# Kernel optimization log

Measured on AMD Instinct MI355X. Metric: run time of the kernel, lower is better.

Reference implementation:

```python
import jax, jax.numpy as jnp
import numpy as np

EPS = 1e-6      # vnn EPS used in norms / leaky-relu denominators
BN_EPS = 1e-5   # torch BatchNorm eps
K = 20          # args.n_knn


def vnlin(W, x):
    # VNLinear: apply (O,C) weight over channel axis 1 of x (B,C,3,...)
    return jnp.moveaxis(jnp.tensordot(W, x, axes=((1,), (1,))), 0, 1)


def vn_bn(x):
    # VNBatchNorm (training-mode batch stats, affine = identity init):
    # normalizes the per-vector norms, rescales vectors accordingly.
    norm = jnp.sqrt(jnp.sum(x * x, axis=2)) + EPS        # (B,C,...)
    axes = (0,) + tuple(range(2, norm.ndim))             # per-channel stats
    mean = jnp.mean(norm, axis=axes, keepdims=True)
    var = jnp.var(norm, axis=axes, keepdims=True)
    norm_bn = (norm - mean) / jnp.sqrt(var + BN_EPS)
    return x / jnp.expand_dims(norm, 2) * jnp.expand_dims(norm_bn, 2)


def vn_lrelu(Wf, Wd, x):
    # VNLinearLeakyReLU with negative_slope=0 (as constructed in this module)
    p = vn_bn(vnlin(Wf, x))
    d = vnlin(Wd, x)
    dot = jnp.sum(p * d, axis=2, keepdims=True)
    dsq = jnp.sum(d * d, axis=2, keepdims=True)
    return jnp.where(dot >= 0, p, p - (dot / (dsq + EPS)) * d)


def vn_maxpool(Wd, x):
    # VNMaxPool: pool over last axis, picking per (b,c) the vector maximizing <x,d>
    d = vnlin(Wd, x)
    dot = jnp.sum(x * d, axis=2, keepdims=True)          # (B,C,1,...)
    idx = jnp.argmax(dot, axis=-1)                       # (B,C,1,...)
    idx = jnp.broadcast_to(idx[..., None], x.shape[:-1] + (1,))
    return jnp.take_along_axis(x, idx, axis=-1)[..., 0]


def graph_feature_cross(x, k):
    # x: (B,3,N) -> (B, 3ch, 3vec, N, k); channels = [nbr-x, x, cross(nbr,x)]
    xx = jnp.sum(x * x, axis=1)                          # (B,N)
    inner = jnp.einsum('bdi,bdj->bij', x, x)             # (B,N,N)
    pd = 2.0 * inner - xx[:, :, None] - xx[:, None, :]   # = -||xi-xj||^2
    idx = jax.lax.top_k(pd, k)[1]                        # (B,N,k) nearest
    pts = jnp.swapaxes(x, 1, 2)                          # (B,N,3)
    nb = jax.vmap(lambda p, i: p[i])(pts, idx)           # (B,N,k,3) gather
    c = jnp.broadcast_to(pts[:, :, None, :], nb.shape)   # center repeated
    cross = jnp.cross(nb, c)
    feat = jnp.stack([nb - c, c, cross], axis=3)         # (B,N,k,3,3)
    return jnp.transpose(feat, (0, 3, 4, 1, 2))


_W_SPECS = {
    'pos_Wf': (21, 3), 'pos_Wd': (21, 3), 'pool_Wd': (21, 21),
    'c1_Wf': (21, 21), 'c1_Wd': (21, 21),
    'st1_Wf': (21, 21), 'st1_Wd': (21, 21),
    'st2_Wf': (42, 21), 'st2_Wd': (42, 21),
    'st3_Wf': (341, 42), 'st3_Wd': (341, 42),
    'st_pool_Wd': (341, 341),
    'stf1_Wf': (170, 341), 'stf1_Wd': (170, 341),
    'stf2_Wf': (85, 170), 'stf2_Wd': (85, 170),
    'stf3_W': (21, 85),
    'c2_Wf': (42, 42), 'c2_Wd': (42, 42),
    'c3_W': (341, 42),
    'std1_Wf': (341, 682), 'std1_Wd': (341, 682),
    'std2_Wf': (170, 341), 'std2_Wd': (170, 341),
    'std_lin': (3, 170),
}


def setup_inputs() -> dict:
    key = jax.random.key(0)
    ks = iter(jax.random.split(key, 32))
    inp = {'x': jax.random.normal(next(ks), (8, 3, 4096), dtype=jnp.float32)}
    for name, (o, i) in _W_SPECS.items():
        inp[name] = jax.random.normal(next(ks), (o, i), dtype=jnp.float32) / np.sqrt(i).astype(np.float32)
    return inp


def _forward(x, pos_Wf, pos_Wd, pool_Wd, c1_Wf, c1_Wd, st1_Wf, st1_Wd, st2_Wf, st2_Wd,
             st3_Wf, st3_Wd, st_pool_Wd, stf1_Wf, stf1_Wd, stf2_Wf, stf2_Wd, stf3_W,
             c2_Wf, c2_Wd, c3_W, std1_Wf, std1_Wd, std2_Wf, std2_Wd, std_lin):
    B, D, N = x.shape
    feat = graph_feature_cross(x, K)                     # (B,3,3,N,k)
    h = vn_lrelu(pos_Wf, pos_Wd, feat)                   # (B,21,3,N,k)
    h = vn_maxpool(pool_Wd, h)                           # (B,21,3,N) pool over k
    h = vn_lrelu(c1_Wf, c1_Wd, h)                        # (B,21,3,N)
    # STNkd feature transform
    s = vn_lrelu(st1_Wf, st1_Wd, h)                      # (B,21,3,N)
    s = vn_lrelu(st2_Wf, st2_Wd, s)                      # (B,42,3,N)
    s = vn_lrelu(st3_Wf, st3_Wd, s)                      # (B,341,3,N)
    s = vn_maxpool(st_pool_Wd, s)                        # (B,341,3) pool over N
    s = vn_lrelu(stf1_Wf, stf1_Wd, s)                    # (B,170,3)
    s = vn_lrelu(stf2_Wf, stf2_Wd, s)                    # (B,85,3)
    s = vnlin(stf3_W, s)                                 # (B,21,3)
    s = jnp.broadcast_to(s[..., None], h.shape)          # repeat over N
    h = jnp.concatenate([h, s], axis=1)                  # (B,42,3,N)
    h = vn_lrelu(c2_Wf, c2_Wd, h)                        # (B,42,3,N)
    h = vn_bn(vnlin(c3_W, h))                            # (B,341,3,N)
    h_mean = jnp.broadcast_to(jnp.mean(h, axis=-1, keepdims=True), h.shape)
    h = jnp.concatenate([h, h_mean], axis=1)             # (B,682,3,N)
    # VNStdFeature (normalize_frame=False)
    z0 = vn_lrelu(std1_Wf, std1_Wd, h)                   # (B,341,3,N)
    z0 = vn_lrelu(std2_Wf, std2_Wd, z0)                  # (B,170,3,N)
    z0 = vnlin(std_lin, z0)                              # (B,3,3,N)
    h_std = jnp.einsum('bijm,bjkm->bikm', h, z0)         # (B,682,3,N)
    out = jnp.max(h_std.reshape(B, -1, N), axis=-1)      # (B,2046)
    return out, z0


def reference(x, pos_Wf, pos_Wd, pool_Wd, c1_Wf, c1_Wd, st1_Wf, st1_Wd, st2_Wf, st2_Wd,
              st3_Wf, st3_Wd, st_pool_Wd, stf1_Wf, stf1_Wd, stf2_Wf, stf2_Wd, stf3_W,
              c2_Wf, c2_Wd, c3_W, std1_Wf, std1_Wd, std2_Wf, std2_Wd, std_lin):
    return _forward(x, pos_Wf, pos_Wd, pool_Wd, c1_Wf, c1_Wd, st1_Wf, st1_Wd, st2_Wf,
                    st2_Wd, st3_Wf, st3_Wd, st_pool_Wd, stf1_Wf, stf1_Wd, stf2_Wf,
                    stf2_Wd, stf3_W, c2_Wf, c2_Wd, c3_W, std1_Wf, std1_Wd, std2_Wf,
                    std2_Wd, std_lin)
```

## Files before the change

kernel.cpp:

```cpp
#include <hip/hip_runtime.h>
#include <cstdint>
#include <cstddef>


typedef unsigned short u16;
using bh8  = __attribute__((ext_vector_type(8))) short;
using f32x4 = __attribute__((ext_vector_type(4))) float;

__device__ __forceinline__ float b2f(u16 v) {
  return __uint_as_float(((unsigned)v) << 16);
}
__device__ __forceinline__ u16 f2b(float f) {
  unsigned u = __float_as_uint(f);
  u += 0x7FFFu + ((u >> 16) & 1u);
  return (u16)(u >> 16);
}

__device__ __forceinline__ float ldg(const float* p, size_t i) { return p[i]; }
__device__ __forceinline__ float ldg(const u16* p, size_t i) { return b2f(p[i]); }
__device__ __forceinline__ void st4(float* p, size_t i, float a, float b, float c, float d) {
  float4 v; v.x = a; v.y = b; v.z = c; v.w = d; *(float4*)(p + i) = v;
}

#define FMA4(A, S, V) { A.x += (S)*(V).x; A.y += (S)*(V).y; A.z += (S)*(V).z; A.w += (S)*(V).w; }

__device__ __forceinline__ unsigned long long packKey(float v, int n) {
  unsigned u = __float_as_uint(v);
  u = (u & 0x80000000u) ? ~u : (u | 0x80000000u);
  return ((unsigned long long)u << 32) | (unsigned long long)(0xFFFFFFFFu - (unsigned)n);
}

#define CSWAP(T) { if (c > T) { unsigned long long tmp = T; T = c; c = tmp; } }
__global__ __launch_bounds__(256) void knn_kernel(const float* __restrict__ x,
                                                  int* __restrict__ idxOut, int N) {
  int b = blockIdx.y;
  int wv = threadIdx.x >> 6, lane = threadIdx.x & 63;
  int i = blockIdx.x * 4 + wv;
  const float* xb = x + (size_t)b * 3 * N;
  float xi0 = xb[i], xi1 = xb[N + i], xi2 = xb[2 * (size_t)N + i];
  float xxi = xi0 * xi0 + xi1 * xi1 + xi2 * xi2;
  unsigned long long t0 = 0, t1 = 0, t2 = 0, t3 = 0, t4 = 0, t5 = 0, t6 = 0, t7 = 0;
  #pragma unroll 8
  for (int s = 0; s < 64; ++s) {
    int j = s * 64 + lane;
    float a0 = xb[j], a1 = xb[N + j], a2 = xb[2 * (size_t)N + j];
    float inner = xi0 * a0 + xi1 * a1 + xi2 * a2;
    float xxj = a0 * a0 + a1 * a1 + a2 * a2;
    float pd = 2.f * inner - xxi - xxj;
    unsigned long long c = packKey(pd, j);
    if (c > t7) { CSWAP(t0) CSWAP(t1) CSWAP(t2) CSWAP(t3) CSWAP(t4) CSWAP(t5) CSWAP(t6) CSWAP(t7) }
  }
  int* row = idxOut + ((size_t)b * N + i) * 20;
  for (int kk = 0; kk < 20; ++kk) {
    unsigned long long k = t0;
    #pragma unroll
    for (int off = 1; off < 64; off <<= 1) {
      unsigned long long o = __shfl_xor(k, off);
      if (o > k) k = o;
    }
    if (lane == 0) row[kk] = (int)(0xFFFFFFFFu - (unsigned)(k & 0xFFFFFFFFull));
    if (k == t0) { t0 = t1; t1 = t2; t2 = t3; t3 = t4; t4 = t5; t5 = t6; t6 = t7; t7 = 0; }
  }
}
#undef CSWAP

__global__ __launch_bounds__(256) void pos_stats(const float* __restrict__ x,
                                                 const int* __restrict__ idx,
                                                 const float* __restrict__ Wf,
                                                 float* __restrict__ statSum,
                                                 float* __restrict__ statSq, int N) {
  __shared__ float wf[64];
  __shared__ float part[4][42];
  int tid = threadIdx.x;
  if (tid < 63) wf[tid] = Wf[tid];
  __syncthreads();
  int b = blockIdx.y;
  int lin = blockIdx.x * 256 + tid;
  int n = lin / 20, kk = lin - n * 20;
  const float* xb = x + (size_t)b * 3 * N;
  int j = idx[((size_t)b * N + n) * 20 + kk];
  float c0 = xb[n], c1 = xb[N + n], c2 = xb[2 * (size_t)N + n];
  float a0 = xb[j], a1 = xb[N + j], a2 = xb[2 * (size_t)N + j];
  float e00 = a0 - c0, e01 = a1 - c1, e02 = a2 - c2;
  float e20 = a1 * c2 - a2 * c1, e21 = a2 * c0 - a0 * c2, e22 = a0 * c1 - a1 * c0;
  int lane = tid & 63, wave = tid >> 6;
  #pragma unroll
  for (int c = 0; c < 21; ++c) {
    float w0 = wf[c * 3], w1 = wf[c * 3 + 1], w2 = wf[c * 3 + 2];
    float p0 = w0 * e00 + w1 * c0 + w2 * e20;
    float p1 = w0 * e01 + w1 * c1 + w2 * e21;
    float p2 = w0 * e02 + w1 * c2 + w2 * e22;
    float nr = sqrtf(p0 * p0 + p1 * p1 + p2 * p2) + 1e-6f;
    float u1 = nr, u2 = nr * nr;
    #pragma unroll
    for (int off = 32; off; off >>= 1) { u1 += __shfl_down(u1, off); u2 += __shfl_down(u2, off); }
    if (lane == 0) { part[wave][c] = u1; part[wave][21 + c] = u2; }
  }
  __syncthreads();
  if (tid < 42) {
    float t = part[0][tid] + part[1][tid] + part[2][tid] + part[3][tid];
    if (tid < 21) atomicAdd(&statSum[tid], t);
    else atomicAdd(&statSq[tid - 21], t);
  }
}

__global__ __launch_bounds__(64) void pos_apply(const float* __restrict__ x,
                                                const int* __restrict__ idx,
                                                const float* __restrict__ Wf,
                                                const float* __restrict__ Wd,
                                                const float* __restrict__ Wpool,
                                                const float* __restrict__ statMean,
                                                const float* __restrict__ statIstd,
                                                float* __restrict__ h0, int N) {
  __shared__ float wpool[441];
  __shared__ float hbuf[64];
  int tid = threadIdx.x;
  for (int l = tid; l < 441; l += 64) wpool[l] = Wpool[l];
  int b = blockIdx.y, n = blockIdx.x;
  bool act = tid < 63;
  int c = act ? tid / 3 : 0;
  int v = act ? tid - c * 3 : 0;
  const float* xb = x + (size_t)b * 3 * N;
  float c0 = xb[n], c1 = xb[N + n], c2 = xb[2 * (size_t)N + n];
  float wf0 = 0, wf1 = 0, wf2 = 0, wd0 = 0, wd1 = 0, wd2 = 0, mn = 0, is = 1.f;
  if (act) {
    wf0 = Wf[c * 3]; wf1 = Wf[c * 3 + 1]; wf2 = Wf[c * 3 + 2];
    wd0 = Wd[c * 3]; wd1 = Wd[c * 3 + 1]; wd2 = Wd[c * 3 + 2];
    mn = statMean[c]; is = statIstd[c];
  }
  __syncthreads();
  float best = -3.4e38f, bh = 0.f;
  const int* idxRow = idx + ((size_t)b * N + n) * 20;
  for (int kk = 0; kk < 20; ++kk) {
    int j = idxRow[kk];
    float a0 = xb[j], a1 = xb[N + j], a2 = xb[2 * (size_t)N + j];
    float av  = (v == 0) ? a0 : ((v == 1) ? a1 : a2);
    float cv  = (v == 0) ? c0 : ((v == 1) ? c1 : c2);
    float a1v = (v == 0) ? a1 : ((v == 1) ? a2 : a0);
    float a2v = (v == 0) ? a2 : ((v == 1) ? a0 : a1);
    float c1v = (v == 0) ? c1 : ((v == 1) ? c2 : c0);
    float c2v = (v == 0) ? c2 : ((v == 1) ? c0 : c1);
    float e0 = av - cv;
    float e1 = cv;
    float e2 = a1v * c2v - a2v * c1v;
    float p = wf0 * e0 + wf1 * e1 + wf2 * e2;
    float d = wd0 * e0 + wd1 * e1 + wd2 * e2;
    int base = c * 3;
    float pp = p * p;
    float n2 = __shfl(pp, base) + __shfl(pp, base + 1) + __shfl(pp, base + 2);
    float nr = sqrtf(n2) + 1e-6f;
    float sc = ((nr - mn) * is) / nr;
    float pb = p * sc;
    float pd2 = pb * d, dd = d * d;
    float dot = __shfl(pd2, base) + __shfl(pd2, base + 1) + __shfl(pd2, base + 2);
    float dsq = __shfl(dd, base) + __shfl(dd, base + 1) + __shfl(dd, base + 2);
    float h = (dot >= 0.f) ? pb : pb - (dot / (dsq + 1e-6f)) * d;
    hbuf[tid] = act ? h : 0.f;
    __syncthreads();
    float d2 = 0.f;
    #pragma unroll 7
    for (int cc = 0; cc < 21; ++cc) d2 += wpool[c * 21 + cc] * hbuf[cc * 3 + v];
    float hd = h * d2;
    float dotp = __shfl(hd, base) + __shfl(hd, base + 1) + __shfl(hd, base + 2);
    if (act && dotp > best) { best = dotp; bh = h; }
    __syncthreads();
  }
  if (act) h0[(((size_t)b * 21 + c) * 3 + v) * N + n] = bh;
}

template<int MODE, int CPT, typename TX, typename TY>
__global__ __launch_bounds__(256) void gemm_vn(
    const float* __restrict__ Wf,
    const TX* __restrict__ X, TY* __restrict__ Y,
    float* __restrict__ statSum, float* __restrict__ statSq,
    const float* __restrict__ statMean, const float* __restrict__ statIstd,
    int Cin, int Cout, int CoutStride, int wstride, int N) {
  __shared__ float Xs[16][3][64];
  __shared__ float Wfs[16 * CPT][17];
  const int tid = threadIdx.x;
  const int tx = tid & 15, ty = tid >> 4;
  const int b = blockIdx.z;
  const int n0 = blockIdx.x * 64;
  const int co0 = blockIdx.y * (16 * CPT);
  const TX* Xb = X + (size_t)b * Cin * 3 * N;

  float4 acc[CPT][3];
  #pragma unroll
  for (int c = 0; c < CPT; ++c)
    #pragma unroll
    for (int v = 0; v < 3; ++v) acc[c][v] = {0.f, 0.f, 0.f, 0.f};

  for (int k0 = 0; k0 < Cin; k0 += 16) {
    #pragma unroll
    for (int l0 = 0; l0 < 12; ++l0) {
      int l = l0 * 256 + tid;
      int n = l & 63, v = (l >> 6) % 3, kk = l / 192;
      int ci = k0 + kk;
      Xs[kk][v][n] = (ci < Cin) ? ldg(Xb, ((size_t)ci * 3 + v) * N + n0 + n) : 0.f;
    }
    {
      int kk = tid & 15, coL = tid >> 4, ci = k0 + kk;
      #pragma unroll
      for (int c = 0; c < CPT; ++c) {
        int co = co0 + coL + 16 * c;
        bool ok = (co < Cout) && (ci < Cin);
        Wfs[coL + 16 * c][kk] = ok ? Wf[(size_t)co * wstride + ci] : 0.f;
      }
    }
    __syncthreads();
    #pragma unroll
    for (int kk = 0; kk < 16; ++kk) {
      float4 x0 = *(const float4*)&Xs[kk][0][tx * 4];
      float4 x1 = *(const float4*)&Xs[kk][1][tx * 4];
      float4 x2 = *(const float4*)&Xs[kk][2][tx * 4];
      #pragma unroll
      for (int c = 0; c < CPT; ++c) {
        float w = Wfs[ty + 16 * c][kk];
        FMA4(acc[c][0], w, x0); FMA4(acc[c][1], w, x1); FMA4(acc[c][2], w, x2);
      }
    }
    __syncthreads();
  }

  #pragma unroll
  for (int c = 0; c < CPT; ++c) {
    int co = co0 + ty + 16 * c;
    float p_[3][4];
    #pragma unroll
    for (int v = 0; v < 3; ++v) {
      const float* av = (const float*)&acc[c][v];
      p_[v][0] = av[0]; p_[v][1] = av[1]; p_[v][2] = av[2]; p_[v][3] = av[3];
    }
    if constexpr (MODE == 5) {
      float s1 = 0.f, s2 = 0.f;
      if (co < Cout) {
        size_t yb = ((size_t)b * CoutStride + co) * 3 * N + n0 + tx * 4;
        #pragma unroll
        for (int j = 0; j < 4; ++j) {
          float nr = sqrtf(p_[0][j]*p_[0][j] + p_[1][j]*p_[1][j] + p_[2][j]*p_[2][j]) + 1e-6f;
          s1 += nr; s2 += nr * nr;
        }
        st4(Y, yb,                 p_[0][0], p_[0][1], p_[0][2], p_[0][3]);
        st4(Y, yb + N,             p_[1][0], p_[1][1], p_[1][2], p_[1][3]);
        st4(Y, yb + 2 * (size_t)N, p_[2][0], p_[2][1], p_[2][2], p_[2][3]);
      }
      #pragma unroll
      for (int off = 8; off; off >>= 1) { s1 += __shfl_down(s1, off); s2 += __shfl_down(s2, off); }
      if (tx == 0 && co < Cout) { atomicAdd(&statSum[co], s1); atomicAdd(&statSq[co], s2); }
    } else if constexpr (MODE == 6) {
      if (co < Cout) {
        float mn = statMean[co], is = statIstd[co];
        size_t yb = ((size_t)b * CoutStride + co) * 3 * N + n0 + tx * 4;
        float4 P0 = *(const float4*)&Y[yb];
        float4 P1 = *(const float4*)&Y[yb + N];
        float4 P2 = *(const float4*)&Y[yb + 2 * (size_t)N];
        float pr[3][4] = {{P0.x,P0.y,P0.z,P0.w},{P1.x,P1.y,P1.z,P1.w},{P2.x,P2.y,P2.z,P2.w}};
        float o_[3][4];
        #pragma unroll
        for (int j = 0; j < 4; ++j) {
          float q0 = pr[0][j], q1 = pr[1][j], q2 = pr[2][j];
          float e0 = p_[0][j], e1 = p_[1][j], e2 = p_[2][j];
          float nr = sqrtf(q0*q0 + q1*q1 + q2*q2) + 1e-6f;
          float sc = ((nr - mn) * is) / nr;
          q0 *= sc; q1 *= sc; q2 *= sc;
          float dot = q0*e0 + q1*e1 + q2*e2;
          if (dot < 0.f) {
            float dsq = e0*e0 + e1*e1 + e2*e2;
            float t = dot / (dsq + 1e-6f);
            q0 -= t*e0; q1 -= t*e1; q2 -= t*e2;
          }
          o_[0][j] = q0; o_[1][j] = q1; o_[2][j] = q2;
        }
        st4(Y, yb,                 o_[0][0], o_[0][1], o_[0][2], o_[0][3]);
        st4(Y, yb + N,             o_[1][0], o_[1][1], o_[1][2], o_[1][3]);
        st4(Y, yb + 2 * (size_t)N, o_[2][0], o_[2][1], o_[2][2], o_[2][3]);
      }
    }
  }
}

__global__ __launch_bounds__(256) void gemm_pool_db(
    const float* __restrict__ Wp, const float* __restrict__ Xp,
    unsigned long long* __restrict__ poolPart, int Cout, int N) {
  constexpr int KP = 352, CPT = 4;
  __shared__ float Xs[2][16][3][64];
  __shared__ float Wfs[2][16 * CPT][16];
  const int tid = threadIdx.x;
  const int tx = tid & 15, ty = tid >> 4;
  const int lane = tid & 63, w = tid >> 6;
  const int b = blockIdx.z;
  const int n0 = blockIdx.x * 64;
  const int co0 = blockIdx.y * (16 * CPT);
  const float* Xb = Xp + (size_t)b * KP * 3 * N;

  auto stage = [&](int k0, int buf) {
    #pragma unroll
    for (int l0 = 0; l0 < 12; ++l0) {
      int q = l0 * 4 + w;
      int vv = q % 3, kk = q / 3;
      const float* g = Xb + ((size_t)(k0 + kk) * 3 + vv) * N + n0 + lane;
      __builtin_amdgcn_global_load_lds(
          (const __attribute__((address_space(1))) float*)g,
          (__attribute__((address_space(3))) float*)&Xs[buf][kk][vv][0], 4, 0, 0);
    }
    #pragma unroll
    for (int c = 0; c < CPT; ++c) {
      const float* g = Wp + (size_t)(co0 + w * 4 + (lane >> 4) + 16 * c) * KP + k0 + (lane & 15);
      __builtin_amdgcn_global_load_lds(
          (const __attribute__((address_space(1))) float*)g,
          (__attribute__((address_space(3))) float*)&Wfs[buf][w * 4 + 16 * c][0], 4, 0, 0);
    }
  };

  float4 acc[CPT][3];
  #pragma unroll
  for (int c = 0; c < CPT; ++c)
    #pragma unroll
    for (int v = 0; v < 3; ++v) acc[c][v] = {0.f, 0.f, 0.f, 0.f};

  stage(0, 0);
  __syncthreads();
  constexpr int KT = KP / 16;
  for (int kt = 0; kt < KT; ++kt) {
    int buf = kt & 1;
    if (kt + 1 < KT) stage((kt + 1) * 16, buf ^ 1);
    #pragma unroll
    for (int kk = 0; kk < 16; ++kk) {
      float4 x0 = *(const float4*)&Xs[buf][kk][0][tx * 4];
      float4 x1 = *(const float4*)&Xs[buf][kk][1][tx * 4];
      float4 x2 = *(const float4*)&Xs[buf][kk][2][tx * 4];
      #pragma unroll
      for (int c = 0; c < CPT; ++c) {
        float wv = Wfs[buf][ty + 16 * c][kk];
        FMA4(acc[c][0], wv, x0); FMA4(acc[c][1], wv, x1); FMA4(acc[c][2], wv, x2);
      }
    }
    __syncthreads();
  }

  #pragma unroll
  for (int c = 0; c < CPT; ++c) {
    int co = co0 + ty + 16 * c;
    unsigned long long key = 0;
    if (co < Cout) {
      const float* av0 = (const float*)&acc[c][0];
      const float* av1 = (const float*)&acc[c][1];
      const float* av2 = (const float*)&acc[c][2];
      size_t xb2 = ((size_t)co * 3) * N + n0 + tx * 4;
      #pragma unroll
      for (int j = 0; j < 4; ++j) {
        float X0 = Xb[xb2 + j];
        float X1 = Xb[xb2 + N + j];
        float X2 = Xb[xb2 + 2 * (size_t)N + j];
        float dot = X0 * av0[j] + X1 * av1[j] + X2 * av2[j];
        unsigned long long k2 = packKey(dot, n0 + tx * 4 + j);
        if (k2 > key) key = k2;
      }
    }
    #pragma unroll
    for (int off = 8; off; off >>= 1) {
      unsigned long long o = __shfl_down(key, off);
      if (o > key) key = o;
    }
    if (tx == 0 && co < Cout) poolPart[((size_t)b * Cout + co) * 64 + blockIdx.x] = key;
  }
}

template<int MODE, int NS>
__global__ __launch_bounds__(256) void mfma2(
    const u16* __restrict__ W, const u16* __restrict__ Xt,
    u16* __restrict__ P, float* __restrict__ Zout,
    const float* __restrict__ biasP, const float* __restrict__ biasD,
    float* __restrict__ statSum, float* __restrict__ statSq,
    const float* __restrict__ statMean, const float* __restrict__ statIstd,
    int Cout, int Cpad, int Kpad, int N) {
  const int tid = threadIdx.x, lane = tid & 63, w = tid >> 6;
  const int quad = lane >> 4, l16 = lane & 15;
  const int b = blockIdx.z, n0 = blockIdx.x * 64, co0 = blockIdx.y * 64;
  const int n = n0 + w * 16 + l16;
  const u16* Xb = Xt + (size_t)b * 3 * N * Kpad;
  f32x4 acc[NS][3];
  #pragma unroll
  for (int s = 0; s < NS; ++s)
    #pragma unroll
    for (int v = 0; v < 3; ++v) acc[s][v] = {0.f, 0.f, 0.f, 0.f};

  for (int k0 = 0; k0 < Kpad; k0 += 32) {
    bh8 bx[3];
    #pragma unroll
    for (int v = 0; v < 3; ++v)
      bx[v] = *(const bh8*)(Xb + ((size_t)v * N + n) * Kpad + k0 + quad * 8);
    #pragma unroll
    for (int s = 0; s < NS; ++s) {
      bh8 a = *(const bh8*)(W + (size_t)(co0 + s * 16 + l16) * Kpad + k0 + quad * 8);
      #pragma unroll
      for (int v = 0; v < 3; ++v)
        acc[s][v] = __builtin_amdgcn_mfma_f32_16x16x32_bf16(a, bx[v], acc[s][v], 0, 0, 0);
    }
  }

  u16* Pb = P + (size_t)b * 3 * N * Cpad;
  #pragma unroll
  for (int s = 0; s < NS; ++s) {
    int cb = co0 + s * 16 + quad * 4;
    if constexpr (MODE == 0) {
      #pragma unroll
      for (int r = 0; r < 4; ++r) {
        int co = cb + r;
        if (co < Cout) {
          size_t zb = (((size_t)b * Cout + co) * 3) * N + n;
          Zout[zb] = acc[s][0][r];
          Zout[zb + N] = acc[s][1][r];
          Zout[zb + 2 * (size_t)N] = acc[s][2][r];
        }
      }
    } else if constexpr (MODE == 1) {
      if (cb < Cpad) {
        float q[3][4];
        #pragma unroll
        for (int r = 0; r < 4; ++r) {
          int co = cb + r;
          float b0 = 0, b1 = 0, b2 = 0;
          if (biasP != nullptr && co < Cout) {
            size_t bi = ((size_t)b * Cout + co) * 3;
            b0 = biasP[bi]; b1 = biasP[bi + 1]; b2 = biasP[bi + 2];
          }
          float q0 = acc[s][0][r] + b0, q1 = acc[s][1][r] + b1, q2 = acc[s][2][r] + b2;
          if (co >= Cout) { q0 = 0.f; q1 = 0.f; q2 = 0.f; }
          q[0][r] = q0; q[1][r] = q1; q[2][r] = q2;
          float nr = sqrtf(q0*q0 + q1*q1 + q2*q2) + 1e-6f;
          float s1 = nr, s2 = nr * nr;
          #pragma unroll
          for (int off = 1; off < 16; off <<= 1) { s1 += __shfl_xor(s1, off); s2 += __shfl_xor(s2, off); }
          if (l16 == 0 && co < Cout) { atomicAdd(&statSum[co], s1); atomicAdd(&statSq[co], s2); }
        }
        #pragma unroll
        for (int v = 0; v < 3; ++v) {
          u16 ob[4];
          ob[0] = f2b(q[v][0]); ob[1] = f2b(q[v][1]); ob[2] = f2b(q[v][2]); ob[3] = f2b(q[v][3]);
          *(ushort4*)(Pb + ((size_t)v * N + n) * Cpad + cb) = *(ushort4*)ob;
        }
      }
    } else {
      if (cb < Cpad) {
        u16 pa[3][4];
        #pragma unroll
        for (int v = 0; v < 3; ++v)
          *(ushort4*)pa[v] = *(const ushort4*)(Pb + ((size_t)v * N + n) * Cpad + cb);
        float o[3][4];
        #pragma unroll
        for (int r = 0; r < 4; ++r) {
          int co = cb + r;
          float r0 = 0.f, r1 = 0.f, r2 = 0.f;
          if (co < Cout) {
            float p0 = b2f(pa[0][r]), p1 = b2f(pa[1][r]), p2 = b2f(pa[2][r]);
            float d0 = acc[s][0][r], d1 = acc[s][1][r], d2 = acc[s][2][r];
            if (biasD != nullptr) {
              size_t bi = ((size_t)b * Cout + co) * 3;
              d0 += biasD[bi]; d1 += biasD[bi + 1]; d2 += biasD[bi + 2];
            }
            float mn = statMean[co], is = statIstd[co];
            float nr = sqrtf(p0*p0 + p1*p1 + p2*p2) + 1e-6f;
            float sc = ((nr - mn) * is) / nr;
            float q0 = p0 * sc, q1 = p1 * sc, q2 = p2 * sc;
            float dot = q0*d0 + q1*d1 + q2*d2;
            if (dot < 0.f) {
              float dsq = d0*d0 + d1*d1 + d2*d2;
              float t = dot / (dsq + 1e-6f);
              q0 -= t*d0; q1 -= t*d1; q2 -= t*d2;
            }
            r0 = q0; r1 = q1; r2 = q2;
          }
          o[0][r] = r0; o[1][r] = r1; o[2][r] = r2;
        }
        #pragma unroll
        for (int v = 0; v < 3; ++v) {
          u16 ob[4];
          ob[0] = f2b(o[v][0]); ob[1] = f2b(o[v][1]); ob[2] = f2b(o[v][2]); ob[3] = f2b(o[v][3]);
          *(ushort4*)(Pb + ((size_t)v * N + n) * Cpad + cb) = *(ushort4*)ob;
        }
      }
    }
  }
}

__global__ void w_to_bf16(const float* __restrict__ W, u16* __restrict__ Wp,
                          int Cout, int Cin, int wstride, int CoutPad, int Kpad) {
  int t = blockIdx.x * 256 + threadIdx.x;
  if (t >= CoutPad * Kpad) return;
  int co = t / Kpad, ci = t - co * Kpad;
  Wp[t] = (co < Cout && ci < Cin) ? f2b(W[(size_t)co * wstride + ci]) : (u16)0;
}

__global__ void w_to_f32pad(const float* __restrict__ W, float* __restrict__ Wp,
                            int Cout, int Cin, int wstride, int CoutPad, int Kpad) {
  int t = blockIdx.x * 256 + threadIdx.x;
  if (t >= CoutPad * Kpad) return;
  int co = t / Kpad, ci = t - co * Kpad;
  Wp[t] = (co < Cout && ci < Cin) ? W[(size_t)co * wstride + ci] : 0.f;
}

__global__ void zero_kernel(float* p, int n) {
  int t = blockIdx.x * 256 + threadIdx.x;
  if (t < n) p[t] = 0.f;
}

__global__ void finalize_kernel(float* __restrict__ sum, float* __restrict__ sq,
                                float* __restrict__ mean, float* __restrict__ istd,
                                int C, float invCount) {
  int c = blockIdx.x * 256 + threadIdx.x;
  if (c < C) {
    float m = sum[c] * invCount;
    float v = sq[c] * invCount - m * m;
    if (v < 0.f) v = 0.f;
    mean[c] = m;
    istd[c] = 1.f / sqrtf(v + 1e-5f);
  }
  if (c < 512) { sum[c] = 0.f; sq[c] = 0.f; }
}

__global__ __launch_bounds__(64) void pool_reduce(const unsigned long long* __restrict__ part,
                                                  const float* __restrict__ s3,
                                                  float* __restrict__ pooled, int N) {
  int co = blockIdx.x, b = blockIdx.y, lane = threadIdx.x;
  unsigned long long key = part[((size_t)b * 341 + co) * 64 + lane];
  #pragma unroll
  for (int off = 32; off; off >>= 1) {
    unsigned long long o = __shfl_down(key, off);
    if (o > key) key = o;
  }
  if (lane == 0) {
    int n = (int)(0xFFFFFFFFu - (unsigned)(key & 0xFFFFFFFFull));
    size_t base = ((size_t)b * 352 + co) * 3;
    size_t obase = ((size_t)b * 341 + co) * 3;
    pooled[obase + 0] = s3[(base + 0) * N + n];
    pooled[obase + 1] = s3[(base + 1) * N + n];
    pooled[obase + 2] = s3[(base + 2) * N + n];
  }
}

__global__ __launch_bounds__(64) void stf_lrelu(const float* __restrict__ Wf,
                                                const float* __restrict__ Wd,
                                                const float* __restrict__ X,
                                                float* __restrict__ Y, int Cin, int Cout) {
  __shared__ float P[24], D[24], NORM[8], SC[8], DOT[8], DSQ[8], MS[2];
  int co = blockIdx.x, tid = threadIdx.x;
  if (tid < 48) {
    int l = tid < 24 ? tid : tid - 24;
    int b = l / 3, v = l - b * 3;
    const float* W = (tid < 24 ? Wf : Wd) + (size_t)co * Cin;
    const float* xb = X + ((size_t)b * Cin) * 3 + v;
    float acc = 0.f;
    for (int ci = 0; ci < Cin; ++ci) acc += W[ci] * xb[ci * 3];
    if (tid < 24) P[l] = acc; else D[l] = acc;
  }
  __syncthreads();
  if (tid < 8) NORM[tid] = sqrtf(P[tid*3]*P[tid*3] + P[tid*3+1]*P[tid*3+1] + P[tid*3+2]*P[tid*3+2]) + 1e-6f;
  __syncthreads();
  if (tid == 0) {
    float m = 0.f;
    for (int b2 = 0; b2 < 8; ++b2) m += NORM[b2];
    m *= 0.125f;
    float var = 0.f;
    for (int b2 = 0; b2 < 8; ++b2) { float dd = NORM[b2] - m; var += dd * dd; }
    var *= 0.125f;
    MS[0] = m; MS[1] = 1.f / sqrtf(var + 1e-5f);
  }
  __syncthreads();
  if (tid < 8) {
    float sc = ((NORM[tid] - MS[0]) * MS[1]) / NORM[tid];
    float dot = 0.f, dsq = 0.f;
    for (int v = 0; v < 3; ++v) {
      float pb = P[tid*3+v] * sc; float dv = D[tid*3+v];
      dot += pb * dv; dsq += dv * dv;
    }
    SC[tid] = sc; DOT[tid] = dot; DSQ[tid] = dsq;
  }
  __syncthreads();
  if (tid < 24) {
    int b = tid / 3;
    float pb = P[tid] * SC[b];
    float o = (DOT[b] >= 0.f) ? pb : pb - (DOT[b] / (DSQ[b] + 1e-6f)) * D[tid];
    Y[((size_t)b * Cout + co) * 3 + (tid - b * 3)] = o;
  }
}

__global__ void vnlin_small(const float* __restrict__ W, const float* __restrict__ X,
                            float* __restrict__ Y, int Cin, int Cout) {
  int t = blockIdx.x * 256 + threadIdx.x;
  if (t >= 8 * Cout * 3) return;
  int v = t % 3, r = t / 3;
  int co = r % Cout, b = r / Cout;
  float acc = 0.f;
  for (int ci = 0; ci < Cin; ++ci) acc += W[(size_t)co * Cin + ci] * X[((size_t)b * Cin + ci) * 3 + v];
  Y[t] = acc;
}

__global__ __launch_bounds__(256) void concat_tt(const float* __restrict__ h1,
                                                 const float* __restrict__ sfin,
                                                 u16* __restrict__ s2bb, int N) {
  __shared__ u16 tile[64][66];
  int b = blockIdx.z, v = blockIdx.y, n0 = blockIdx.x * 64;
  int tn = threadIdx.x & 63, tc = threadIdx.x >> 6;
  for (int c = tc; c < 64; c += 4) {
    u16 val = 0;
    if (c < 21) val = f2b(h1[(((size_t)b * 21 + c) * 3 + v) * N + n0 + tn]);
    else if (c < 42) val = f2b(sfin[((size_t)b * 21 + (c - 21)) * 3 + v]);
    tile[c][tn] = val;
  }
  __syncthreads();
  u16* dst = s2bb + (((size_t)b * 3 + v) * N + n0) * 64;
  for (int n = tc; n < 64; n += 4)
    dst[(size_t)n * 64 + tn] = tile[tn][n];
}

__global__ __launch_bounds__(384) void bn_apply_mean(u16* __restrict__ H,
    const float* __restrict__ sMean, const float* __restrict__ sIstd,
    float* __restrict__ HmAcc, int N) {
  int c = threadIdx.x;
  if (c >= 341) return;
  int b = blockIdx.y, nt = blockIdx.x;
  float mn = sMean[c], is = sIstd[c];
  float a0 = 0.f, a1 = 0.f, a2 = 0.f;
  size_t base = (size_t)b * 3 * N * 352;
  for (int n = nt * 64; n < nt * 64 + 64; ++n) {
    size_t i0 = base + ((size_t)0 * N + n) * 352 + c;
    size_t i1 = base + ((size_t)1 * N + n) * 352 + c;
    size_t i2 = base + ((size_t)2 * N + n) * 352 + c;
    float p0 = b2f(H[i0]), p1 = b2f(H[i1]), p2 = b2f(H[i2]);
    float nr = sqrtf(p0*p0 + p1*p1 + p2*p2) + 1e-6f;
    float sc = ((nr - mn) * is) / nr;
    p0 *= sc; p1 *= sc; p2 *= sc;
    H[i0] = f2b(p0); H[i1] = f2b(p1); H[i2] = f2b(p2);
    a0 += p0; a1 += p1; a2 += p2;
  }
  size_t hb = ((size_t)b * 341 + c) * 3;
  atomicAdd(&HmAcc[hb], a0); atomicAdd(&HmAcc[hb + 1], a1); atomicAdd(&HmAcc[hb + 2], a2);
}

__global__ void hm_finalize(float* Hm, float invN) {
  int t = blockIdx.x * 256 + threadIdx.x;
  if (t < 8 * 341 * 3) Hm[t] *= invN;
}

__global__ void bias_kernel(const float* __restrict__ Wf, const float* __restrict__ Wd,
                            const float* __restrict__ Hm,
                            float* __restrict__ biasP, float* __restrict__ biasD) {
  int t = blockIdx.x * 256 + threadIdx.x;
  if (t >= 8 * 341 * 3) return;
  int v = t % 3, r = t / 3;
  int co = r % 341, b = r / 341;
  const float* hm = Hm + (size_t)b * 1023 + v;
  float ap = 0.f, ad = 0.f;
  for (int j = 0; j < 341; ++j) {
    float h = hm[j * 3];
    ap += Wf[(size_t)co * 682 + 341 + j] * h;
    ad += Wd[(size_t)co * 682 + 341 + j] * h;
  }
  biasP[t] = ap; biasD[t] = ad;
}

__global__ __launch_bounds__(256) void final_max_part(const u16* __restrict__ H,
    const float* __restrict__ Hm, const float* __restrict__ z0,
    float* __restrict__ part, int N, int NT) {
  __shared__ float red[3][4][64];
  int b = blockIdx.z, nt = blockIdx.y;
  int il = threadIdx.x & 63, nsub = threadIdx.x >> 6;
  int i = blockIdx.x * 64 + il;
  bool valid = i < 682, lo = i < 341;
  float c0 = 0, c1 = 0, c2 = 0;
  if (valid && !lo) {
    size_t hb = ((size_t)b * 341 + (i - 341)) * 3;
    c0 = Hm[hb]; c1 = Hm[hb + 1]; c2 = Hm[hb + 2];
  }
  const float* zb = z0 + (size_t)b * 9 * N;
  const u16* Hb = H + (size_t)b * 3 * N * 352;
  float m0 = -3.4e38f, m1 = -3.4e38f, m2 = -3.4e38f;
  int ii = lo ? i : 0;
  int chunk = N / NT, nBeg = nt * chunk;
  for (int n = nBeg + nsub; n < nBeg + chunk; n += 4) {
    float a0, a1, a2;
    if (lo) {
      a0 = b2f(Hb[((size_t)0 * N + n) * 352 + ii]);
      a1 = b2f(Hb[((size_t)1 * N + n) * 352 + ii]);
      a2 = b2f(Hb[((size_t)2 * N + n) * 352 + ii]);
    } else { a0 = c0; a1 = c1; a2 = c2; }
    float s0 = a0 * zb[n]                + a1 * zb[3 * (size_t)N + n] + a2 * zb[6 * (size_t)N + n];
    float s1 = a0 * zb[N + n]            + a1 * zb[4 * (size_t)N + n] + a2 * zb[7 * (size_t)N + n];
    float s2 = a0 * zb[2 * (size_t)N + n]+ a1 * zb[5 * (size_t)N + n] + a2 * zb[8 * (size_t)N + n];
    m0 = fmaxf(m0, s0); m1 = fmaxf(m1, s1); m2 = fmaxf(m2, s2);
  }
  red[0][nsub][il] = m0; red[1][nsub][il] = m1; red[2][nsub][il] = m2;
  __syncthreads();
  if (nsub == 0 && valid) {
    for (int q = 1; q < 4; ++q) {
      m0 = fmaxf(m0, red[0][q][il]); m1 = fmaxf(m1, red[1][q][il]); m2 = fmaxf(m2, red[2][q][il]);
    }
    size_t pb = ((size_t)b * 682 + i) * 3;
    part[(pb + 0) * NT + nt] = m0;
    part[(pb + 1) * NT + nt] = m1;
    part[(pb + 2) * NT + nt] = m2;
  }
}

__global__ void final_max_reduce(const float* __restrict__ part,
                                 float* __restrict__ out, int NT) {
  int t = blockIdx.x * 256 + threadIdx.x;
  if (t >= 8 * 682 * 3) return;
  const float* p = part + (size_t)t * NT;
  float m = p[0];
  for (int k = 1; k < NT; ++k) m = fmaxf(m, p[k]);
  out[t] = m;
}

extern "C" void kernel_launch(void* const* d_in, const int* in_sizes, int n_in,
                              void* d_out, int out_size, void* d_ws, size_t ws_size,
                              hipStream_t stream) {
  (void)in_sizes; (void)n_in; (void)out_size; (void)ws_size;
  const float* x       = (const float*)d_in[0];
  const float* pos_Wf  = (const float*)d_in[1];
  const float* pos_Wd  = (const float*)d_in[2];
  const float* pool_Wd = (const float*)d_in[3];
  const float* c1_Wf   = (const float*)d_in[4];
  const float* c1_Wd   = (const float*)d_in[5];
  const float* st1_Wf  = (const float*)d_in[6];
  const float* st1_Wd  = (const float*)d_in[7];
  const float* st2_Wf  = (const float*)d_in[8];
  const float* st2_Wd  = (const float*)d_in[9];
  const float* st3_Wf  = (const float*)d_in[10];
  const float* st3_Wd  = (const float*)d_in[11];
  const float* stp_Wd  = (const float*)d_in[12];
  const float* stf1_Wf = (const float*)d_in[13];
  const float* stf1_Wd = (const float*)d_in[14];
  const float* stf2_Wf = (const float*)d_in[15];
  const float* stf2_Wd = (const float*)d_in[16];
  const float* stf3_W  = (const float*)d_in[17];
  const float* c2_Wf   = (const float*)d_in[18];
  const float* c2_Wd   = (const float*)d_in[19];
  const float* c3_W    = (const float*)d_in[20];
  const float* std1_Wf = (const float*)d_in[21];
  const float* std1_Wd = (const float*)d_in[22];
  const float* std2_Wf = (const float*)d_in[23];
  const float* std2_Wd = (const float*)d_in[24];
  const float* stdlin  = (const float*)d_in[25];

  float* outv  = (float*)d_out;
  float* z0out = outv + 8 * 2046;

  const int N = 4096;
  const int NT = 32;
  char* ws = (char*)d_ws;
  size_t off = 0;
  auto alloc = [&](size_t bytes) -> char* {
    char* p = ws + off;
    off += (bytes + 255) & ~(size_t)255;
    return p;
  };
  float* stats = (float*)alloc(2048 * sizeof(float));
  float* sSum = stats, *sSq = stats + 512, *sMean = stats + 1024, *sIstd = stats + 1536;
  int* idx = (int*)alloc((size_t)8 * N * 20 * 4);
  unsigned long long* poolPart = (unsigned long long*)alloc((size_t)8 * 341 * 64 * 8);
  float* fmPart = (float*)alloc((size_t)8 * 682 * 3 * NT * 4);
  float* Wpoolp = (float*)alloc((size_t)384 * 352 * 4);
  float* pooled = (float*)alloc(8 * 341 * 3 * 4);
  float* stf1o  = (float*)alloc(8 * 170 * 3 * 4);
  float* stf2o  = (float*)alloc(8 * 85 * 3 * 4);
  float* sfin   = (float*)alloc(8 * 21 * 3 * 4);
  float* Hm     = (float*)alloc(8 * 1023 * 4);
  float* biasP  = (float*)alloc(8 * 341 * 3 * 4);
  float* biasD  = (float*)alloc(8 * 341 * 3 * 4);
  const size_t E21 = (size_t)8 * 21 * 3 * N, E42 = (size_t)8 * 42 * 3 * N;
  const size_t T352 = (size_t)8 * 3 * N * 352 * 2;
  const size_t T192 = (size_t)8 * 3 * N * 192 * 2;
  const size_t T64  = (size_t)8 * 3 * N * 64 * 2;
  const size_t F352 = (size_t)8 * 352 * 3 * N * 4;
  char* regionA = alloc(T352);
  char* regionB = alloc(F352);
  float* h0  = (float*)regionA;
  float* h1  = h0 + E21;
  float* s1b = h0 + 2 * E21;
  float* s2b = h0 + 3 * E21;
  float* st3o = (float*)regionB;
  u16* Hbuf  = (u16*)regionB;
  u16* Pstd2 = (u16*)(regionB + T352);
  u16* s2bb  = (u16*)(regionB + T352 + T192);
  u16* h2b   = (u16*)(regionB + T352 + T192 + T64);
  u16* Pstd1 = (u16*)regionA;
  u16* W1fp = (u16*)poolPart;
  u16* W1dp = W1fp + 384 * 352;
  u16* W2fp = W1dp + 384 * 352;
  u16* W2dp = W2fp + 192 * 352;
  u16* Wc3p = W2dp + 192 * 352;
  u16* Wc2f = Wc3p + 384 * 64;
  u16* Wc2d = Wc2f + 64 * 64;
  u16* Wzp  = Wc2d + 64 * 64;

  dim3 blk256(256), blk64(64);
  auto run_lrelu32 = [&](const float* Wf, const float* Wd, const float* X, float* Y,
                         int Cin, int Cout, int CoutStride, int wstride, float invCnt) {
    dim3 grid(64, (Cout + 31) / 32, 8);
    gemm_vn<5, 2><<<grid, blk256, 0, stream>>>(Wf, X, Y, sSum, sSq,
                                               nullptr, nullptr, Cin, Cout, CoutStride, wstride, N);
    finalize_kernel<<<dim3(2), blk256, 0, stream>>>(sSum, sSq, sMean, sIstd, Cout, invCnt);
    gemm_vn<6, 2><<<grid, blk256, 0, stream>>>(Wd, X, Y, nullptr, nullptr,
                                               sMean, sIstd, Cin, Cout, CoutStride, wstride, N);
  };
  const float invBN = 1.f / (8.f * N);
  auto run_mfma = [&](const u16* Wf, const u16* Wd, const u16* X, u16* P,
                      const float* bP, const float* bD,
                      int Cout, int Cpad, int Kpad, int coTiles) {
    dim3 grid(64, coTiles, 8);
    mfma2<1, 4><<<grid, blk256, 0, stream>>>(Wf, X, P, nullptr, bP, nullptr,
                                             sSum, sSq, nullptr, nullptr, Cout, Cpad, Kpad, N);
    finalize_kernel<<<dim3(2), blk256, 0, stream>>>(sSum, sSq, sMean, sIstd, Cout, invBN);
    mfma2<2, 4><<<grid, blk256, 0, stream>>>(Wd, X, P, nullptr, nullptr, bD,
                                             nullptr, nullptr, sMean, sIstd, Cout, Cpad, Kpad, N);
  };

  zero_kernel<<<dim3(4), blk256, 0, stream>>>(stats, 1024);
  w_to_f32pad<<<dim3((384 * 352 + 255) / 256), blk256, 0, stream>>>(stp_Wd, Wpoolp, 341, 341, 341, 384, 352);
  knn_kernel<<<dim3(N / 4, 8), blk256, 0, stream>>>(x, idx, N);
  pos_stats<<<dim3(N * 20 / 256, 8), blk256, 0, stream>>>(x, idx, pos_Wf, sSum, sSq, N);
  finalize_kernel<<<dim3(2), blk256, 0, stream>>>(sSum, sSq, sMean, sIstd, 21, 1.f / (8.f * N * 20.f));
  pos_apply<<<dim3(N, 8), blk64, 0, stream>>>(x, idx, pos_Wf, pos_Wd, pool_Wd, sMean, sIstd, h0, N);

  run_lrelu32(c1_Wf, c1_Wd, h0, h1, 21, 21, 21, 21, invBN);
  run_lrelu32(st1_Wf, st1_Wd, h1, s1b, 21, 21, 21, 21, invBN);
  run_lrelu32(st2_Wf, st2_Wd, s1b, s2b, 21, 42, 42, 21, invBN);
  run_lrelu32(st3_Wf, st3_Wd, s2b, st3o, 42, 341, 352, 42, invBN);

  gemm_pool_db<<<dim3(64, 6, 8), blk256, 0, stream>>>(Wpoolp, st3o, poolPart, 341, N);
  pool_reduce<<<dim3(341, 8), blk64, 0, stream>>>(poolPart, st3o, pooled, N);

  w_to_bf16<<<dim3((384 * 352 + 255) / 256), blk256, 0, stream>>>(std1_Wf, W1fp, 341, 341, 682, 384, 352);
  w_to_bf16<<<dim3((384 * 352 + 255) / 256), blk256, 0, stream>>>(std1_Wd, W1dp, 341, 341, 682, 384, 352);
  w_to_bf16<<<dim3((192 * 352 + 255) / 256), blk256, 0, stream>>>(std2_Wf, W2fp, 170, 341, 341, 192, 352);
  w_to_bf16<<<dim3((192 * 352 + 255) / 256), blk256, 0, stream>>>(std2_Wd, W2dp, 170, 341, 341, 192, 352);
  w_to_bf16<<<dim3((384 * 64 + 255) / 256), blk256, 0, stream>>>(c3_W, Wc3p, 341, 42, 42, 384, 64);
  w_to_bf16<<<dim3((64 * 64 + 255) / 256), blk256, 0, stream>>>(c2_Wf, Wc2f, 42, 42, 42, 64, 64);
  w_to_bf16<<<dim3((64 * 64 + 255) / 256), blk256, 0, stream>>>(c2_Wd, Wc2d, 42, 42, 42, 64, 64);
  w_to_bf16<<<dim3((16 * 192 + 255) / 256), blk256, 0, stream>>>(stdlin, Wzp, 3, 170, 170, 16, 192);

  stf_lrelu<<<dim3(170), blk64, 0, stream>>>(stf1_Wf, stf1_Wd, pooled, stf1o, 341, 170);
  stf_lrelu<<<dim3(85),  blk64, 0, stream>>>(stf2_Wf, stf2_Wd, stf1o, stf2o, 170, 85);
  vnlin_small<<<dim3(2), blk256, 0, stream>>>(stf3_W, stf2o, sfin, 85, 21);

  concat_tt<<<dim3(N / 64, 3, 8), blk256, 0, stream>>>(h1, sfin, s2bb, N);
  run_mfma(Wc2f, Wc2d, s2bb, h2b, nullptr, nullptr, 42, 64, 64, 1);

  {
    dim3 grid(64, 6, 8);
    mfma2<1, 4><<<grid, blk256, 0, stream>>>(Wc3p, h2b, Hbuf, nullptr, nullptr, nullptr,
                                             sSum, sSq, nullptr, nullptr, 341, 352, 64, N);
  }
  finalize_kernel<<<dim3(2), blk256, 0, stream>>>(sSum, sSq, sMean, sIstd, 341, invBN);
  zero_kernel<<<dim3(32), blk256, 0, stream>>>(Hm, 8 * 1023);
  bn_apply_mean<<<dim3(64, 8), dim3(384), 0, stream>>>(Hbuf, sMean, sIstd, Hm, N);
  hm_finalize<<<dim3(32), blk256, 0, stream>>>(Hm, 1.f / (float)N);
  bias_kernel<<<dim3(32), blk256, 0, stream>>>(std1_Wf, std1_Wd, Hm, biasP, biasD);

  run_mfma(W1fp, W1dp, Hbuf, Pstd1, biasP, biasD, 341, 352, 352, 6);
  run_mfma(W2fp, W2dp, Pstd1, Pstd2, nullptr, nullptr, 170, 192, 352, 3);

  mfma2<0, 1><<<dim3(64, 1, 8), blk256, 0, stream>>>(Wzp, Pstd2, nullptr, z0out,
                                                     nullptr, nullptr, nullptr, nullptr,
                                                     nullptr, nullptr, 3, 16, 192, N);
  final_max_part<<<dim3(11, NT, 8), blk256, 0, stream>>>(Hbuf, Hm, z0out, fmPart, N, NT);
  final_max_reduce<<<dim3((8 * 682 * 3 + 255) / 256), blk256, 0, stream>>>(fmPart, outv, NT);
}
```

Measured before the change: 2.690 ms.

## Replace VN linear GEMMs with double-buffered async LDS loads over padded channels

```diff
diff --git a/kernel.cpp b/kernel.cpp
--- a/kernel.cpp
+++ b/kernel.cpp
@@ -16,8 +16,6 @@
   return (u16)(u >> 16);
 }
 
-__device__ __forceinline__ float ldg(const float* p, size_t i) { return p[i]; }
-__device__ __forceinline__ float ldg(const u16* p, size_t i) { return b2f(p[i]); }
 __device__ __forceinline__ void st4(float* p, size_t i, float a, float b, float c, float d) {
   float4 v; v.x = a; v.y = b; v.z = c; v.w = d; *(float4*)(p + i) = v;
 }
@@ -165,24 +163,53 @@
     if (act && dotp > best) { best = dotp; bh = h; }
     __syncthreads();
   }
-  if (act) h0[(((size_t)b * 21 + c) * 3 + v) * N + n] = bh;
-}
-
-template<int MODE, int CPT, typename TX, typename TY>
-__global__ __launch_bounds__(256) void gemm_vn(
-    const float* __restrict__ Wf,
-    const TX* __restrict__ X, TY* __restrict__ Y,
+  if (act) h0[(((size_t)b * 32 + c) * 3 + v) * N + n] = bh;
+}
+
+__global__ void zero_padch(float* __restrict__ p, int Cfrom, int Cpad, int N) {
+  size_t t = (size_t)blockIdx.x * 256 + threadIdx.x;
+  size_t per = (size_t)(Cpad - Cfrom) * 3 * N;
+  if (t >= 8 * per) return;
+  int b = (int)(t / per);
+  size_t r = t - (size_t)b * per;
+  p[(((size_t)b * Cpad + Cfrom) * 3) * N + r] = 0.f;
+}
+
+template<int MODE, int CPT>
+__global__ __launch_bounds__(256) void gemm_db(
+    const float* __restrict__ Wp, const float* __restrict__ Xp,
+    float* __restrict__ Yp,
     float* __restrict__ statSum, float* __restrict__ statSq,
     const float* __restrict__ statMean, const float* __restrict__ statIstd,
-    int Cin, int Cout, int CoutStride, int wstride, int N) {
-  __shared__ float Xs[16][3][64];
-  __shared__ float Wfs[16 * CPT][17];
+    int Cout, int CpadY, int Kpad, int N) {
+  __shared__ float Xs[2][16][3][64];
+  __shared__ float Wfs[2][16 * CPT][16];
   const int tid = threadIdx.x;
   const int tx = tid & 15, ty = tid >> 4;
+  const int lane = tid & 63, w = tid >> 6;
   const int b = blockIdx.z;
   const int n0 = blockIdx.x * 64;
   const int co0 = blockIdx.y * (16 * CPT);
-  const TX* Xb = X + (size_t)b * Cin * 3 * N;
+  const float* Xb = Xp + (size_t)b * Kpad * 3 * N;
+
+  auto stage = [&](int k0, int buf) {
+    #pragma unroll
+    for (int l0 = 0; l0 < 12; ++l0) {
+      int q = l0 * 4 + w;
+      int vv = q % 3, kk = q / 3;
+      const float* g = Xb + ((size_t)(k0 + kk) * 3 + vv) * N + n0 + lane;
+      __builtin_amdgcn_global_load_lds(
+          (const __attribute__((address_space(1))) float*)g,
+          (__attribute__((address_space(3))) float*)&Xs[buf][kk][vv][0], 4, 0, 0);
+    }
+    #pragma unroll
+    for (int c = 0; c < CPT; ++c) {
+      const float* g = Wp + (size_t)(co0 + w * 4 + (lane >> 4) + 16 * c) * Kpad + k0 + (lane & 15);
+      __builtin_amdgcn_global_load_lds(
+          (const __attribute__((address_space(1))) float*)g,
+          (__attribute__((address_space(3))) float*)&Wfs[buf][w * 4 + 16 * c][0], 4, 0, 0);
+    }
+  };
 
   float4 acc[CPT][3];
   #pragma unroll
@@ -190,33 +217,21 @@
     #pragma unroll
     for (int v = 0; v < 3; ++v) acc[c][v] = {0.f, 0.f, 0.f, 0.f};
 
-  for (int k0 = 0; k0 < Cin; k0 += 16) {
-    #pragma unroll
-    for (int l0 = 0; l0 < 12; ++l0) {
-      int l = l0 * 256 + tid;
-      int n = l & 63, v = (l >> 6) % 3, kk = l / 192;
-      int ci = k0 + kk;
-      Xs[kk][v][n] = (ci < Cin) ? ldg(Xb, ((size_t)ci * 3 + v) * N + n0 + n) : 0.f;
-    }
-    {
-      int kk = tid & 15, coL = tid >> 4, ci = k0 + kk;
+  stage(0, 0);
+  __syncthreads();
+  const int KT = Kpad / 16;
+  for (int kt = 0; kt < KT; ++kt) {
+    int buf = kt & 1;
+    if (kt + 1 < KT) stage((kt + 1) * 16, buf ^ 1);
+    #pragma unroll
+    for (int kk = 0; kk < 16; ++kk) {
+      float4 x0 = *(const float4*)&Xs[buf][kk][0][tx * 4];
+      float4 x1 = *(const float4*)&Xs[buf][kk][1][tx * 4];
+      float4 x2 = *(const float4*)&Xs[buf][kk][2][tx * 4];
       #pragma unroll
       for (int c = 0; c < CPT; ++c) {
-        int co = co0 + coL + 16 * c;
-        bool ok = (co < Cout) && (ci < Cin);
-        Wfs[coL + 16 * c][kk] = ok ? Wf[(size_t)co * wstride + ci] : 0.f;
-      }
-    }
-    __syncthreads();
-    #pragma unroll
-    for (int kk = 0; kk < 16; ++kk) {
-      float4 x0 = *(const float4*)&Xs[kk][0][tx * 4];
-      float4 x1 = *(const float4*)&Xs[kk][1][tx * 4];
-      float4 x2 = *(const float4*)&Xs[kk][2][tx * 4];
-      #pragma unroll
-      for (int c = 0; c < CPT; ++c) {
-        float w = Wfs[ty + 16 * c][kk];
-        FMA4(acc[c][0], w, x0); FMA4(acc[c][1], w, x1); FMA4(acc[c][2], w, x2);
+        float wv = Wfs[buf][ty + 16 * c][kk];
+        FMA4(acc[c][0], wv, x0); FMA4(acc[c][1], wv, x1); FMA4(acc[c][2], wv, x2);
       }
     }
     __syncthreads();
@@ -225,41 +240,36 @@
   #pragma unroll
   for (int c = 0; c < CPT; ++c) {
     int co = co0 + ty + 16 * c;
-    float p_[3][4];
-    #pragma unroll
-    for (int v = 0; v < 3; ++v) {
-      const float* av = (const float*)&acc[c][v];
-      p_[v][0] = av[0]; p_[v][1] = av[1]; p_[v][2] = av[2]; p_[v][3] = av[3];
-    }
+    if (co >= CpadY) continue;
+    const float* a0 = (const float*)&acc[c][0];
+    const float* a1 = (const float*)&acc[c][1];
+    const float* a2 = (const float*)&acc[c][2];
+    size_t yb = ((size_t)b * CpadY + co) * 3 * N + n0 + tx * 4;
     if constexpr (MODE == 5) {
       float s1 = 0.f, s2 = 0.f;
-      if (co < Cout) {
-        size_t yb = ((size_t)b * CoutStride + co) * 3 * N + n0 + tx * 4;
-        #pragma unroll
-        for (int j = 0; j < 4; ++j) {
-          float nr = sqrtf(p_[0][j]*p_[0][j] + p_[1][j]*p_[1][j] + p_[2][j]*p_[2][j]) + 1e-6f;
-          s1 += nr; s2 += nr * nr;
-        }
-        st4(Y, yb,                 p_[0][0], p_[0][1], p_[0][2], p_[0][3]);
-        st4(Y, yb + N,             p_[1][0], p_[1][1], p_[1][2], p_[1][3]);
-        st4(Y, yb + 2 * (size_t)N, p_[2][0], p_[2][1], p_[2][2], p_[2][3]);
+      #pragma unroll
+      for (int j = 0; j < 4; ++j) {
+        float nr = sqrtf(a0[j]*a0[j] + a1[j]*a1[j] + a2[j]*a2[j]) + 1e-6f;
+        s1 += nr; s2 += nr * nr;
       }
+      st4(Yp, yb,                 a0[0], a0[1], a0[2], a0[3]);
+      st4(Yp, yb + N,             a1[0], a1[1], a1[2], a1[3]);
+      st4(Yp, yb + 2 * (size_t)N, a2[0], a2[1], a2[2], a2[3]);
       #pragma unroll
       for (int off = 8; off; off >>= 1) { s1 += __shfl_down(s1, off); s2 += __shfl_down(s2, off); }
       if (tx == 0 && co < Cout) { atomicAdd(&statSum[co], s1); atomicAdd(&statSq[co], s2); }
-    } else if constexpr (MODE == 6) {
+    } else {
       if (co < Cout) {
         float mn = statMean[co], is = statIstd[co];
-        size_t yb = ((size_t)b * CoutStride + co) * 3 * N + n0 + tx * 4;
-        float4 P0 = *(const float4*)&Y[yb];
-        float4 P1 = *(const float4*)&Y[yb + N];
-        float4 P2 = *(const float4*)&Y[yb + 2 * (size_t)N];
+        float4 P0 = *(const float4*)&Yp[yb];
+        float4 P1 = *(const float4*)&Yp[yb + N];
+        float4 P2 = *(const float4*)&Yp[yb + 2 * (size_t)N];
         float pr[3][4] = {{P0.x,P0.y,P0.z,P0.w},{P1.x,P1.y,P1.z,P1.w},{P2.x,P2.y,P2.z,P2.w}};
         float o_[3][4];
         #pragma unroll
         for (int j = 0; j < 4; ++j) {
           float q0 = pr[0][j], q1 = pr[1][j], q2 = pr[2][j];
-          float e0 = p_[0][j], e1 = p_[1][j], e2 = p_[2][j];
+          float e0 = a0[j], e1 = a1[j], e2 = a2[j];
           float nr = sqrtf(q0*q0 + q1*q1 + q2*q2) + 1e-6f;
           float sc = ((nr - mn) * is) / nr;
           q0 *= sc; q1 *= sc; q2 *= sc;
@@ -271,9 +281,13 @@
           }
           o_[0][j] = q0; o_[1][j] = q1; o_[2][j] = q2;
         }
-        st4(Y, yb,                 o_[0][0], o_[0][1], o_[0][2], o_[0][3]);
-        st4(Y, yb + N,             o_[1][0], o_[1][1], o_[1][2], o_[1][3]);
-        st4(Y, yb + 2 * (size_t)N, o_[2][0], o_[2][1], o_[2][2], o_[2][3]);
+        st4(Yp, yb,                 o_[0][0], o_[0][1], o_[0][2], o_[0][3]);
+        st4(Yp, yb + N,             o_[1][0], o_[1][1], o_[1][2], o_[1][3]);
+        st4(Yp, yb + 2 * (size_t)N, o_[2][0], o_[2][1], o_[2][2], o_[2][3]);
+      } else {
+        st4(Yp, yb, 0.f, 0.f, 0.f, 0.f);
+        st4(Yp, yb + N, 0.f, 0.f, 0.f, 0.f);
+        st4(Yp, yb + 2 * (size_t)N, 0.f, 0.f, 0.f, 0.f);
       }
     }
   }
@@ -604,7 +618,7 @@
   int tn = threadIdx.x & 63, tc = threadIdx.x >> 6;
   for (int c = tc; c < 64; c += 4) {
     u16 val = 0;
-    if (c < 21) val = f2b(h1[(((size_t)b * 21 + c) * 3 + v) * N + n0 + tn]);
+    if (c < 21) val = f2b(h1[(((size_t)b * 32 + c) * 3 + v) * N + n0 + tn]);
     else if (c < 42) val = f2b(sfin[((size_t)b * 21 + (c - 21)) * 3 + v]);
     tile[c][tn] = val;
   }
@@ -762,6 +776,14 @@
   unsigned long long* poolPart = (unsigned long long*)alloc((size_t)8 * 341 * 64 * 8);
   float* fmPart = (float*)alloc((size_t)8 * 682 * 3 * NT * 4);
   float* Wpoolp = (float*)alloc((size_t)384 * 352 * 4);
+  float* Wc1f = (float*)alloc(32 * 32 * 4);
+  float* Wc1d = (float*)alloc(32 * 32 * 4);
+  float* Ws1f = (float*)alloc(32 * 32 * 4);
+  float* Ws1d = (float*)alloc(32 * 32 * 4);
+  float* Ws2f = (float*)alloc(64 * 32 * 4);
+  float* Ws2d = (float*)alloc(64 * 32 * 4);
+  float* Ws3f = (float*)alloc(352 * 48 * 4);
+  float* Ws3d = (float*)alloc(352 * 48 * 4);
   float* pooled = (float*)alloc(8 * 341 * 3 * 4);
   float* stf1o  = (float*)alloc(8 * 170 * 3 * 4);
   float* stf2o  = (float*)alloc(8 * 85 * 3 * 4);
@@ -769,7 +791,8 @@
   float* Hm     = (float*)alloc(8 * 1023 * 4);
   float* biasP  = (float*)alloc(8 * 341 * 3 * 4);
   float* biasD  = (float*)alloc(8 * 341 * 3 * 4);
-  const size_t E21 = (size_t)8 * 21 * 3 * N, E42 = (size_t)8 * 42 * 3 * N;
+  const size_t P32 = (size_t)8 * 32 * 3 * N;
+  const size_t P48 = (size_t)8 * 48 * 3 * N;
   const size_t T352 = (size_t)8 * 3 * N * 352 * 2;
   const size_t T192 = (size_t)8 * 3 * N * 192 * 2;
   const size_t T64  = (size_t)8 * 3 * N * 64 * 2;
@@ -777,9 +800,9 @@
   char* regionA = alloc(T352);
   char* regionB = alloc(F352);
   float* h0  = (float*)regionA;
-  float* h1  = h0 + E21;
-  float* s1b = h0 + 2 * E21;
-  float* s2b = h0 + 3 * E21;
+  float* h1  = h0 + P32;
+  float* s1b = h1 + P32;
+  float* s2b = s1b + P32;
   float* st3o = (float*)regionB;
   u16* Hbuf  = (u16*)regionB;
   u16* Pstd2 = (u16*)(regionB + T352);
@@ -796,16 +819,16 @@
   u16* Wzp  = Wc2d + 64 * 64;
 
   dim3 blk256(256), blk64(64);
-  auto run_lrelu32 = [&](const float* Wf, const float* Wd, const float* X, float* Y,
-                         int Cin, int Cout, int CoutStride, int wstride, float invCnt) {
-    dim3 grid(64, (Cout + 31) / 32, 8);
-    gemm_vn<5, 2><<<grid, blk256, 0, stream>>>(Wf, X, Y, sSum, sSq,
-                                               nullptr, nullptr, Cin, Cout, CoutStride, wstride, N);
+  const float invBN = 1.f / (8.f * N);
+  auto run_db = [&](const float* Wfp, const float* Wdp, const float* X, float* Y,
+                    int Cout, int CpadY, int Kpad, int coTiles, float invCnt) {
+    dim3 grid(64, coTiles, 8);
+    gemm_db<5, 2><<<grid, blk256, 0, stream>>>(Wfp, X, Y, sSum, sSq, nullptr, nullptr,
+                                               Cout, CpadY, Kpad, N);
     finalize_kernel<<<dim3(2), blk256, 0, stream>>>(sSum, sSq, sMean, sIstd, Cout, invCnt);
-    gemm_vn<6, 2><<<grid, blk256, 0, stream>>>(Wd, X, Y, nullptr, nullptr,
-                                               sMean, sIstd, Cin, Cout, CoutStride, wstride, N);
+    gemm_db<6, 2><<<grid, blk256, 0, stream>>>(Wdp, X, Y, nullptr, nullptr, sMean, sIstd,
+                                               Cout, CpadY, Kpad, N);
   };
-  const float invBN = 1.f / (8.f * N);
   auto run_mfma = [&](const u16* Wf, const u16* Wd, const u16* X, u16* P,
                       const float* bP, const float* bD,
                       int Cout, int Cpad, int Kpad, int coTiles) {
@@ -819,15 +842,25 @@
 
   zero_kernel<<<dim3(4), blk256, 0, stream>>>(stats, 1024);
   w_to_f32pad<<<dim3((384 * 352 + 255) / 256), blk256, 0, stream>>>(stp_Wd, Wpoolp, 341, 341, 341, 384, 352);
+  w_to_f32pad<<<dim3((32 * 32 + 255) / 256), blk256, 0, stream>>>(c1_Wf, Wc1f, 21, 21, 21, 32, 32);
+  w_to_f32pad<<<dim3((32 * 32 + 255) / 256), blk256, 0, stream>>>(c1_Wd, Wc1d, 21, 21, 21, 32, 32);
+  w_to_f32pad<<<dim3((32 * 32 + 255) / 256), blk256, 0, stream>>>(st1_Wf, Ws1f, 21, 21, 21, 32, 32);
+  w_to_f32pad<<<dim3((32 * 32 + 255) / 256), blk256, 0, stream>>>(st1_Wd, Ws1d, 21, 21, 21, 32, 32);
+  w_to_f32pad<<<dim3((64 * 32 + 255) / 256), blk256, 0, stream>>>(st2_Wf, Ws2f, 42, 21, 21, 64, 32);
+  w_to_f32pad<<<dim3((64 * 32 + 255) / 256), blk256, 0, stream>>>(st2_Wd, Ws2d, 42, 21, 21, 64, 32);
+  w_to_f32pad<<<dim3((352 * 48 + 255) / 256), blk256, 0, stream>>>(st3_Wf, Ws3f, 341, 42, 42, 352, 48);
+  w_to_f32pad<<<dim3((352 * 48 + 255) / 256), blk256, 0, stream>>>(st3_Wd, Ws3d, 341, 42, 42, 352, 48);
+  zero_padch<<<dim3((8 * 11 * 3 * N + 255) / 256), blk256, 0, stream>>>(h0, 21, 32, N);
+
   knn_kernel<<<dim3(N / 4, 8), blk256, 0, stream>>>(x, idx, N);
   pos_stats<<<dim3(N * 20 / 256, 8), blk256, 0, stream>>>(x, idx, pos_Wf, sSum, sSq, N);
   finalize_kernel<<<dim3(2), blk256, 0, stream>>>(sSum, sSq, sMean, sIstd, 21, 1.f / (8.f * N * 20.f));
   pos_apply<<<dim3(N, 8), blk64, 0, stream>>>(x, idx, pos_Wf, pos_Wd, pool_Wd, sMean, sIstd, h0, N);
 
-  run_lrelu32(c1_Wf, c1_Wd, h0, h1, 21, 21, 21, 21, invBN);
-  run_lrelu32(st1_Wf, st1_Wd, h1, s1b, 21, 21, 21, 21, invBN);
-  run_lrelu32(st2_Wf, st2_Wd, s1b, s2b, 21, 42, 42, 21, invBN);
-  run_lrelu32(st3_Wf, st3_Wd, s2b, st3o, 42, 341, 352, 42, invBN);
+  run_db(Wc1f, Wc1d, h0, h1, 21, 32, 32, 1, invBN);
+  run_db(Ws1f, Ws1d, h1, s1b, 21, 32, 32, 1, invBN);
+  run_db(Ws2f, Ws2d, s1b, s2b, 42, 48, 32, 2, invBN);
+  run_db(Ws3f, Ws3d, s2b, st3o, 341, 352, 48, 11, invBN);
 
   gemm_pool_db<<<dim3(64, 6, 8), blk256, 0, stream>>>(Wpoolp, st3o, poolPart, 341, N);
   pool_reduce<<<dim3(341, 8), blk64, 0, stream>>>(poolPart, st3o, pooled, N);
```

After: 2.684 ms. Within noise of the previous version (-0.2%).
